# Kernel optimization log

Measured on AMD Instinct MI355X. Metric: run time of the kernel, lower is better.

## Reference

```python
import jax, jax.numpy as jnp
import numpy as np

# Polynomial coefficients from the original module (hard-coded in forward).
P00, P10, P20, P30 = 0.0, 0.0, 0.0, 0.0      # identity-kernel branch (all zero)
P01, P11, P21 = -0.000287, 0.266, -0.1097    # learned-weight branch
STRIDE, PAD = 1, 1


def _conv(x, w):
    # NCHW input, OIHW kernel -> NCHW output. Equivalent to
    # unfold(x).T @ w.view(O,-1).T reshaped back, i.e. torch's im2col matmul.
    return jax.lax.conv_general_dilated(
        x, w,
        window_strides=(STRIDE, STRIDE),
        padding=[(PAD, PAD), (PAD, PAD)],
        dimension_numbers=('NCHW', 'OIHW', 'NCHW'))


def setup_inputs() -> dict:
    key = jax.random.key(0)
    k1, k2 = jax.random.split(key)
    img = jax.random.normal(k1, (16, 64, 128, 128), dtype=jnp.float32)
    # weights initialized N(0, 0.8) in the original module
    weights = jax.random.normal(k2, (64, 64, 3, 3), dtype=jnp.float32) * 0.8
    identity_kernel = jnp.ones((64, 64, 3, 3), dtype=jnp.float32)
    return {"img": img, "weights": weights, "identity_kernel": identity_kernel}


def reference(img, weights, identity_kernel):
    kh, kw = weights.shape[2], weights.shape[3]
    # Elementwise polynomial applied to the input, then contracted against
    # the (identity, learned) kernels. matmul-with-unfold == convolution,
    # so we express it as two convs instead of materializing im2col.
    poly_id = P00 + P10 * img + P20 * img**2 + P30 * img**3  # == zeros here
    poly_w = P01 + P11 * img + P21 * img**2
    out = _conv(poly_id, identity_kernel) + _conv(poly_w, weights)
    return out / (3 * kh * kw)
```

## Files before the change

### kernel.cpp

```cpp
#include <hip/hip_runtime.h>


typedef __bf16 bf16;
typedef __attribute__((ext_vector_type(8))) __bf16 bf16x8;
typedef __attribute__((ext_vector_type(16))) float f32x16;

static constexpr float A0 = -0.000287f / 27.0f;
static constexpr float A1 =  0.266f    / 27.0f;
static constexpr float A2 = -0.1097f   / 27.0f;

#define NN 16
#define CI 64
#define HH 128
#define WW 128
#define OO 64

__global__ void repack_w(const float* __restrict__ w, bf16* __restrict__ wrb) {
    int idx = blockIdx.x * 256 + threadIdx.x;
    if (idx >= 9 * 8 * 64 * 8) return;
    int cj    = idx & 7;
    int o     = (idx >> 3) & 63;
    int cc8   = (idx >> 9) & 7;
    int slice = idx >> 12;
    int ky = slice / 3, kx = slice - ky * 3;
    int c = cc8 * 8 + cj;
    wrb[idx] = (bf16)w[((o * CI + c) * 3 + ky) * 3 + kx];
}

__global__ __launch_bounds__(256) void conv_mfma(const float* __restrict__ img,
                                                 const bf16* __restrict__ wrb,
                                                 float* __restrict__ out) {
    __shared__ __align__(16) bf16 ilds[4 * 8 * 130 * 8];

    const int tid = threadIdx.x;
    const int b   = blockIdx.x;
    const int y0  = (b & 63) * 2;
    const int n   = b >> 6;

    for (int t = tid; t < 4 * 8 * 130; t += 256) {
        int r   = t / (8 * 130);
        int rem = t - r * (8 * 130);
        int cc8 = rem / 130;
        int xp  = rem - cc8 * 130;
        int yi  = y0 - 1 + r;
        int xi  = xp - 1;
        bf16x8 pk;
        if ((unsigned)yi < 128u && (unsigned)xi < 128u) {
            const float* p = img + ((n * CI + cc8 * 8) * HH + yi) * WW + xi;
            #pragma unroll
            for (int j = 0; j < 8; ++j) {
                float v = p[j * HH * WW];
                pk[j] = (bf16)(A0 + v * (A1 + A2 * v));
            }
        } else {
            #pragma unroll
            for (int j = 0; j < 8; ++j) pk[j] = (bf16)0.0f;
        }
        *(bf16x8*)&ilds[t * 8] = pk;
    }
    __syncthreads();

    const int wv   = tid >> 6;
    const int lane = tid & 63;
    const int lm   = lane & 31;
    const int half = lane >> 5;
    const int yl   = wv >> 1;
    const int Xh   = (wv & 1) * 64;

    f32x16 acc[2][2];
    #pragma unroll
    for (int i = 0; i < 2; ++i)
        #pragma unroll
        for (int j = 0; j < 2; ++j)
            #pragma unroll
            for (int k = 0; k < 16; ++k) acc[i][j][k] = 0.0f;

    const bf16x8* wfr = (const bf16x8*)wrb;
    const bf16x8* ifr = (const bf16x8*)ilds;

    for (int ky = 0; ky < 3; ++ky) {
        const int r = yl + ky;
        #pragma unroll
        for (int kx = 0; kx < 3; ++kx) {
            const int slice = ky * 3 + kx;
            #pragma unroll
            for (int cs = 0; cs < 8; cs += 2) {
                const int cc = cs + half;
                bf16x8 a0 = wfr[(slice * 8 + cc) * 64 + lm];
                bf16x8 a1 = wfr[(slice * 8 + cc) * 64 + 32 + lm];
                const int ibase = (r * 8 + cc) * 130 + Xh + lm + kx;
                bf16x8 b0 = ifr[ibase];
                bf16x8 b1 = ifr[ibase + 32];
                acc[0][0] = __builtin_amdgcn_mfma_f32_32x32x16_bf16(a0, b0, acc[0][0], 0, 0, 0);
                acc[0][1] = __builtin_amdgcn_mfma_f32_32x32x16_bf16(a0, b1, acc[0][1], 0, 0, 0);
                acc[1][0] = __builtin_amdgcn_mfma_f32_32x32x16_bf16(a1, b0, acc[1][0], 0, 0, 0);
                acc[1][1] = __builtin_amdgcn_mfma_f32_32x32x16_bf16(a1, b1, acc[1][1], 0, 0, 0);
            }
        }
    }

    const int y = y0 + yl;
    #pragma unroll
    for (int ot = 0; ot < 2; ++ot) {
        #pragma unroll
        for (int xt = 0; xt < 2; ++xt) {
            const int x = Xh + xt * 32 + lm;
            #pragma unroll
            for (int rg = 0; rg < 16; ++rg) {
                const int o = ot * 32 + (rg & 3) + 8 * (rg >> 2) + 4 * half;
                out[((n * OO + o) * HH + y) * WW + x] = acc[ot][xt][rg];
            }
        }
    }
}

extern "C" void kernel_launch(void* const* d_in, const int* in_sizes, int n_in,
                              void* d_out, int out_size, void* d_ws, size_t ws_size,
                              hipStream_t stream) {
    const float* img = (const float*)d_in[0];
    const float* w   = (const float*)d_in[1];
    float* out = (float*)d_out;
    bf16* wrb  = (bf16*)d_ws;

    repack_w<<<(9 * 8 * 64 * 8 + 255) / 256, 256, 0, stream>>>(w, wrb);
    conv_mfma<<<NN * (HH / 2), 256, 0, stream>>>(img, wrb, out);
}
```

Measured before the change: 138.2 us.

## Double-buffer input channel chunks and process four output rows per block

```diff
diff --git a/kernel.cpp b/kernel.cpp
--- a/kernel.cpp
+++ b/kernel.cpp
@@ -27,38 +27,15 @@
     wrb[idx] = (bf16)w[((o * CI + c) * 3 + ky) * 3 + kx];
 }
 
-__global__ __launch_bounds__(256) void conv_mfma(const float* __restrict__ img,
-                                                 const bf16* __restrict__ wrb,
-                                                 float* __restrict__ out) {
-    __shared__ __align__(16) bf16 ilds[4 * 8 * 130 * 8];
+__global__ __launch_bounds__(512, 4) void conv_mfma(const float* __restrict__ img,
+                                                    const bf16* __restrict__ wrb,
+                                                    float* __restrict__ out) {
+    __shared__ __align__(16) bf16 ilds[2][6 * 2 * 130 * 8];
 
     const int tid = threadIdx.x;
     const int b   = blockIdx.x;
-    const int y0  = (b & 63) * 2;
-    const int n   = b >> 6;
-
-    for (int t = tid; t < 4 * 8 * 130; t += 256) {
-        int r   = t / (8 * 130);
-        int rem = t - r * (8 * 130);
-        int cc8 = rem / 130;
-        int xp  = rem - cc8 * 130;
-        int yi  = y0 - 1 + r;
-        int xi  = xp - 1;
-        bf16x8 pk;
-        if ((unsigned)yi < 128u && (unsigned)xi < 128u) {
-            const float* p = img + ((n * CI + cc8 * 8) * HH + yi) * WW + xi;
-            #pragma unroll
-            for (int j = 0; j < 8; ++j) {
-                float v = p[j * HH * WW];
-                pk[j] = (bf16)(A0 + v * (A1 + A2 * v));
-            }
-        } else {
-            #pragma unroll
-            for (int j = 0; j < 8; ++j) pk[j] = (bf16)0.0f;
-        }
-        *(bf16x8*)&ilds[t * 8] = pk;
-    }
-    __syncthreads();
+    const int y0  = (b & 31) * 4;
+    const int n   = b >> 5;
 
     const int wv   = tid >> 6;
     const int lane = tid & 63;
@@ -66,6 +43,31 @@
     const int half = lane >> 5;
     const int yl   = wv >> 1;
     const int Xh   = (wv & 1) * 64;
+
+    auto stage = [&](int chunk, int buf) {
+        const int cbase = chunk * 16;
+        for (int t = tid; t < 6 * 2 * 130; t += 512) {
+            int r   = t / 260;
+            int rem = t - r * 260;
+            int ccl = rem / 130;
+            int xp  = rem - ccl * 130;
+            int yi  = y0 - 1 + r;
+            int xi  = xp - 1;
+            bf16x8 pk;
+            if ((unsigned)yi < 128u && (unsigned)xi < 128u) {
+                const float* p = img + ((n * CI + cbase + ccl * 8) * HH + yi) * WW + xi;
+                #pragma unroll
+                for (int j = 0; j < 8; ++j) {
+                    float v = p[j * HH * WW];
+                    pk[j] = (bf16)(A0 + v * (A1 + A2 * v));
+                }
+            } else {
+                #pragma unroll
+                for (int j = 0; j < 8; ++j) pk[j] = (bf16)0.0f;
+            }
+            *(bf16x8*)&ilds[buf][((r * 2 + ccl) * 130 + xp) * 8] = pk;
+        }
+    };
 
     f32x16 acc[2][2];
     #pragma unroll
@@ -76,21 +78,25 @@
             for (int k = 0; k < 16; ++k) acc[i][j][k] = 0.0f;
 
     const bf16x8* wfr = (const bf16x8*)wrb;
-    const bf16x8* ifr = (const bf16x8*)ilds;
 
-    for (int ky = 0; ky < 3; ++ky) {
-        const int r = yl + ky;
+    stage(0, 0);
+
+    for (int chunk = 0; chunk < 4; ++chunk) {
+        __syncthreads();
+        if (chunk < 3) stage(chunk + 1, (chunk + 1) & 1);
+        const bf16x8* ifr = (const bf16x8*)ilds[chunk & 1];
+        const int cc8g = chunk * 2 + half;
         #pragma unroll
-        for (int kx = 0; kx < 3; ++kx) {
-            const int slice = ky * 3 + kx;
+        for (int ky = 0; ky < 3; ++ky) {
+            const int r = yl + ky;
             #pragma unroll
-            for (int cs = 0; cs < 8; cs += 2) {
-                const int cc = cs + half;
-                bf16x8 a0 = wfr[(slice * 8 + cc) * 64 + lm];
-                bf16x8 a1 = wfr[(slice * 8 + cc) * 64 + 32 + lm];
-                const int ibase = (r * 8 + cc) * 130 + Xh + lm + kx;
-                bf16x8 b0 = ifr[ibase];
-                bf16x8 b1 = ifr[ibase + 32];
+            for (int kx = 0; kx < 3; ++kx) {
+                const int slice = ky * 3 + kx;
+                bf16x8 a0 = wfr[(slice * 8 + cc8g) * 64 + lm];
+                bf16x8 a1 = wfr[(slice * 8 + cc8g) * 64 + 32 + lm];
+                const int ib = (r * 2 + half) * 130 + Xh + lm + kx;
+                bf16x8 b0 = ifr[ib];
+                bf16x8 b1 = ifr[ib + 32];
                 acc[0][0] = __builtin_amdgcn_mfma_f32_32x32x16_bf16(a0, b0, acc[0][0], 0, 0, 0);
                 acc[0][1] = __builtin_amdgcn_mfma_f32_32x32x16_bf16(a0, b1, acc[0][1], 0, 0, 0);
                 acc[1][0] = __builtin_amdgcn_mfma_f32_32x32x16_bf16(a1, b0, acc[1][0], 0, 0, 0);
@@ -123,5 +129,5 @@
     bf16* wrb  = (bf16*)d_ws;
 
     repack_w<<<(9 * 8 * 64 * 8 + 255) / 256, 256, 0, stream>>>(w, wrb);
-    conv_mfma<<<NN * (HH / 2), 256, 0, stream>>>(img, wrb, out);
+    conv_mfma<<<NN * (HH / 4), 512, 0, stream>>>(img, wrb, out);
 }
```

After: 132.5 us. 1.04x faster.

## Precompute padded bf16 polynomial image and read conv operands directly from global

Applied to the files above, without the earlier changes.

```diff
diff --git a/kernel.cpp b/kernel.cpp
--- a/kernel.cpp
+++ b/kernel.cpp
@@ -14,6 +14,45 @@
 #define HH 128
 #define WW 128
 #define OO 64
+#define HW (HH * WW)
+#define PW 130
+#define PPLANE (PW * PW)
+
+__global__ __launch_bounds__(256) void poly_pack(const float* __restrict__ img,
+                                                 bf16x8* __restrict__ pimg) {
+    const int t = blockIdx.x * 256 + threadIdx.x;
+    if (t < (1 << 21)) {
+        const int x   = t & 127;
+        const int y   = (t >> 7) & 127;
+        const int cc8 = (t >> 14) & 7;
+        const int n   = t >> 17;
+        const float* p = img + ((n * CI + cc8 * 8) * HH + y) * WW + x;
+        bf16x8 pk;
+        #pragma unroll
+        for (int j = 0; j < 8; ++j) {
+            float v = p[j * HW];
+            pk[j] = (bf16)(A0 + v * (A1 + A2 * v));
+        }
+        pimg[(n * 8 + cc8) * PPLANE + (y + 1) * PW + (x + 1)] = pk;
+    } else {
+        int p = t - (1 << 21);
+        const int nc = p / 516;
+        int pi = p - nc * 516;
+        int yp, xp;
+        if (pi < 260) {
+            yp = (pi < 130) ? 0 : 129;
+            xp = (pi < 130) ? pi : pi - 130;
+        } else {
+            int q = pi - 260;
+            xp = (q < 128) ? 0 : 129;
+            yp = ((q < 128) ? q : q - 128) + 1;
+        }
+        bf16x8 z;
+        #pragma unroll
+        for (int j = 0; j < 8; ++j) z[j] = (bf16)0.0f;
+        pimg[nc * PPLANE + yp * PW + xp] = z;
+    }
+}
 
 __global__ void repack_w(const float* __restrict__ w, bf16* __restrict__ wrb) {
     int idx = blockIdx.x * 256 + threadIdx.x;
@@ -27,90 +66,50 @@
     wrb[idx] = (bf16)w[((o * CI + c) * 3 + ky) * 3 + kx];
 }
 
-__global__ __launch_bounds__(256) void conv_mfma(const float* __restrict__ img,
-                                                 const bf16* __restrict__ wrb,
-                                                 float* __restrict__ out) {
-    __shared__ __align__(16) bf16 ilds[4 * 8 * 130 * 8];
+__global__ __launch_bounds__(256, 4) void conv_mfma(const bf16x8* __restrict__ pimg,
+                                                    const bf16x8* __restrict__ wfr,
+                                                    float* __restrict__ out) {
+    const int g   = blockIdx.x;
+    const int xcd = g & 7;
+    const int idx = g >> 3;
+    const int y   = xcd * 16 + (idx & 15);
+    const int n   = idx >> 4;
 
-    const int tid = threadIdx.x;
-    const int b   = blockIdx.x;
-    const int y0  = (b & 63) * 2;
-    const int n   = b >> 6;
-
-    for (int t = tid; t < 4 * 8 * 130; t += 256) {
-        int r   = t / (8 * 130);
-        int rem = t - r * (8 * 130);
-        int cc8 = rem / 130;
-        int xp  = rem - cc8 * 130;
-        int yi  = y0 - 1 + r;
-        int xi  = xp - 1;
-        bf16x8 pk;
-        if ((unsigned)yi < 128u && (unsigned)xi < 128u) {
-            const float* p = img + ((n * CI + cc8 * 8) * HH + yi) * WW + xi;
-            #pragma unroll
-            for (int j = 0; j < 8; ++j) {
-                float v = p[j * HH * WW];
-                pk[j] = (bf16)(A0 + v * (A1 + A2 * v));
-            }
-        } else {
-            #pragma unroll
-            for (int j = 0; j < 8; ++j) pk[j] = (bf16)0.0f;
-        }
-        *(bf16x8*)&ilds[t * 8] = pk;
-    }
-    __syncthreads();
-
+    const int tid  = threadIdx.x;
     const int wv   = tid >> 6;
     const int lane = tid & 63;
     const int lm   = lane & 31;
     const int half = lane >> 5;
-    const int yl   = wv >> 1;
-    const int Xh   = (wv & 1) * 64;
+    const int x0   = wv * 32;
 
-    f32x16 acc[2][2];
+    const bf16x8* vb = pimg + ((n * 8 + half) * PPLANE + y * PW + x0 + lm);
+
+    f32x16 acc0, acc1;
     #pragma unroll
-    for (int i = 0; i < 2; ++i)
-        #pragma unroll
-        for (int j = 0; j < 2; ++j)
-            #pragma unroll
-            for (int k = 0; k < 16; ++k) acc[i][j][k] = 0.0f;
+    for (int k = 0; k < 16; ++k) { acc0[k] = 0.0f; acc1[k] = 0.0f; }
 
-    const bf16x8* wfr = (const bf16x8*)wrb;
-    const bf16x8* ifr = (const bf16x8*)ilds;
-
+    #pragma unroll
     for (int ky = 0; ky < 3; ++ky) {
-        const int r = yl + ky;
         #pragma unroll
         for (int kx = 0; kx < 3; ++kx) {
             const int slice = ky * 3 + kx;
             #pragma unroll
-            for (int cs = 0; cs < 8; cs += 2) {
-                const int cc = cs + half;
-                bf16x8 a0 = wfr[(slice * 8 + cc) * 64 + lm];
-                bf16x8 a1 = wfr[(slice * 8 + cc) * 64 + 32 + lm];
-                const int ibase = (r * 8 + cc) * 130 + Xh + lm + kx;
-                bf16x8 b0 = ifr[ibase];
-                bf16x8 b1 = ifr[ibase + 32];
-                acc[0][0] = __builtin_amdgcn_mfma_f32_32x32x16_bf16(a0, b0, acc[0][0], 0, 0, 0);
-                acc[0][1] = __builtin_amdgcn_mfma_f32_32x32x16_bf16(a0, b1, acc[0][1], 0, 0, 0);
-                acc[1][0] = __builtin_amdgcn_mfma_f32_32x32x16_bf16(a1, b0, acc[1][0], 0, 0, 0);
-                acc[1][1] = __builtin_amdgcn_mfma_f32_32x32x16_bf16(a1, b1, acc[1][1], 0, 0, 0);
+            for (int ccp = 0; ccp < 4; ++ccp) {
+                bf16x8 b = vb[(ccp * 2) * PPLANE + ky * PW + kx];
+                bf16x8 a0 = wfr[(slice * 8 + ccp * 2 + half) * 64 + lm];
+                bf16x8 a1 = wfr[(slice * 8 + ccp * 2 + half) * 64 + 32 + lm];
+                acc0 = __builtin_amdgcn_mfma_f32_32x32x16_bf16(a0, b, acc0, 0, 0, 0);
+                acc1 = __builtin_amdgcn_mfma_f32_32x32x16_bf16(a1, b, acc1, 0, 0, 0);
             }
         }
     }
 
-    const int y = y0 + yl;
+    float* op = out + (n * OO * HH + y) * WW + x0 + lm;
     #pragma unroll
-    for (int ot = 0; ot < 2; ++ot) {
-        #pragma unroll
-        for (int xt = 0; xt < 2; ++xt) {
-            const int x = Xh + xt * 32 + lm;
-            #pragma unroll
-            for (int rg = 0; rg < 16; ++rg) {
-                const int o = ot * 32 + (rg & 3) + 8 * (rg >> 2) + 4 * half;
-                out[((n * OO + o) * HH + y) * WW + x] = acc[ot][xt][rg];
-            }
-        }
+    for (int rg = 0; rg < 16; ++rg) {
+        const int o = (rg & 3) + 8 * (rg >> 2) + 4 * half;
+        op[o * HW]        = acc0[rg];
+        op[(o + 32) * HW] = acc1[rg];
     }
 }
 
@@ -120,8 +119,11 @@
     const float* img = (const float*)d_in[0];
     const float* w   = (const float*)d_in[1];
     float* out = (float*)d_out;
-    bf16* wrb  = (bf16*)d_ws;
 
+    bf16x8* pimg = (bf16x8*)d_ws;
+    bf16*   wrb  = (bf16*)((char*)d_ws + (size_t)NN * 8 * PPLANE * 16);
+
+    poly_pack<<<8450, 256, 0, stream>>>(img, pimg);
     repack_w<<<(9 * 8 * 64 * 8 + 255) / 256, 256, 0, stream>>>(w, wrb);
-    conv_mfma<<<NN * (HH / 2), 256, 0, stream>>>(img, wrb, out);
+    conv_mfma<<<NN * HH, 256, 0, stream>>>(pimg, (const bf16x8*)wrb, out);
 }
```

Result: slower. 149.4 us (+8.1%).
